# Kernel tuning notes

Hardware: AMD Instinct MI355X
Metric: run time of the kernel (lower is better)

The kernel has to match this reference:

```python
import jax, jax.numpy as jnp
import numpy as np

L_GNN = 4          # num_layers - 1
NUM_GRAPHS = 64
BN_EPS = 1e-5


def _bn(x, g, b):
    # torch BatchNorm1d in training mode: biased variance, per-feature affine
    m = x.mean(axis=0)
    v = ((x - m) ** 2).mean(axis=0)
    return g * (x - m) * jax.lax.rsqrt(v + BN_EPS) + b


def _mlp(x, W1, b1, g, bb, W2, b2):
    # GIN 2-layer MLP: Linear -> BN -> ReLU -> Linear
    h = jax.nn.relu(_bn(x @ W1 + b1, g, bb))
    return h @ W2 + b2


def setup_inputs():
    key = jax.random.key(0)
    ks = jax.random.split(key, 20)
    N1, N2, E1, E2 = 8192, 4096, 262144, 65536
    D1, D2, H, O = 128, 64, 512, 10

    def nrm(k, shape, scale=0.05):
        return (jax.random.normal(k, shape) * scale).astype(jnp.float32)

    return {
        "x1": jax.random.normal(ks[0], (N1, D1), jnp.float32),
        "x2": jax.random.normal(ks[1], (N2, D2), jnp.float32),
        "motif2A": jax.random.uniform(ks[2], (N2, N1), jnp.float32),
        "edge1": jax.random.randint(ks[3], (2, E1), 0, N1),
        "edge2": jax.random.randint(ks[4], (2, E2), 0, N2),
        "graph_ids": jnp.sort(jax.random.randint(ks[5], (N1,), 0, NUM_GRAPHS)),
        "eps": jnp.zeros((L_GNN,), jnp.float32),
        "atts": jax.random.uniform(ks[6], (2,), jnp.float32),
        "mlp1_W1_0": nrm(ks[7], (D1, H)),
        "mlp1_W1_rest": nrm(ks[8], (L_GNN - 1, 2 * H, H)),
        "mlp1_b1": jnp.zeros((L_GNN, H), jnp.float32),
        "mlp1_bn_g": jnp.ones((L_GNN, H), jnp.float32),
        "mlp1_bn_b": jnp.zeros((L_GNN, H), jnp.float32),
        "mlp1_W2": nrm(ks[9], (L_GNN, H, H)),
        "mlp1_b2": jnp.zeros((L_GNN, H), jnp.float32),
        "bn1_g": jnp.ones((L_GNN, H), jnp.float32),
        "bn1_b": jnp.zeros((L_GNN, H), jnp.float32),
        "mlp2_W1_0": nrm(ks[10], (D2, H)),
        "mlp2_W1_rest": nrm(ks[11], (L_GNN - 1, H, H)),
        "mlp2_b1": jnp.zeros((L_GNN, H), jnp.float32),
        "mlp2_bn_g": jnp.ones((L_GNN, H), jnp.float32),
        "mlp2_bn_b": jnp.zeros((L_GNN, H), jnp.float32),
        "mlp2_W2": nrm(ks[12], (L_GNN, H, H)),
        "mlp2_b2": jnp.zeros((L_GNN, H), jnp.float32),
        "bn2_g": jnp.ones((L_GNN, H), jnp.float32),
        "bn2_b": jnp.zeros((L_GNN, H), jnp.float32),
        "pred_W0": nrm(ks[13], (D1, O)),
        "pred_b0": jnp.zeros((O,), jnp.float32),
        "pred_W": nrm(ks[14], (L_GNN, 2 * H, O)),
        "pred_b": jnp.zeros((L_GNN, O), jnp.float32),
    }


def reference(x1, x2, motif2A, edge1, edge2, graph_ids, eps, atts,
              mlp1_W1_0, mlp1_W1_rest, mlp1_b1, mlp1_bn_g, mlp1_bn_b, mlp1_W2, mlp1_b2,
              bn1_g, bn1_b,
              mlp2_W1_0, mlp2_W1_rest, mlp2_b1, mlp2_bn_g, mlp2_bn_b, mlp2_W2, mlp2_b2,
              bn2_g, bn2_b,
              pred_W0, pred_b0, pred_W, pred_b):
    N1, N2 = x1.shape[0], x2.shape[0]
    a = jax.nn.softmax(atts)                      # attention over [self-graph, hyper-graph]
    h1, h2 = x1, x2
    hidden = [x1]
    for l in range(L_GNN):
        # spmm(Adj, h) == scatter-sum of source features onto destination rows
        pooled1 = jax.ops.segment_sum(h1[edge1[1]], edge1[0], num_segments=N1)
        pooled1 = pooled1 + (1.0 + eps[l]) * h1   # learn_eps branch (next_layer_eps)
        W1 = mlp1_W1_0 if l == 0 else mlp1_W1_rest[l - 1]
        rep1 = _mlp(pooled1, W1, mlp1_b1[l], mlp1_bn_g[l], mlp1_bn_b[l], mlp1_W2[l], mlp1_b2[l])
        h1 = jax.nn.relu(_bn(rep1, bn1_g[l], bn1_b[l]))
        # hyper graph branch
        pooled2 = jax.ops.segment_sum(h2[edge2[1]], edge2[0], num_segments=N2)
        pooled2 = pooled2 + (1.0 + eps[l]) * h2
        W1h = mlp2_W1_0 if l == 0 else mlp2_W1_rest[l - 1]
        rep2 = _mlp(pooled2, W1h, mlp2_b1[l], mlp2_bn_g[l], mlp2_bn_b[l], mlp2_W2[l], mlp2_b2[l])
        h2 = jax.nn.relu(_bn(rep2, bn2_g[l], bn2_b[l]))
        # project hyper-node features back to base nodes and fuse with attention
        h2A = motif2A.T @ h2                      # [N1, H]
        h1 = jnp.concatenate([a[0] * h1, a[1] * h2A], axis=1)  # [N1, 2H]
        hidden.append(h1)
    # jumping-knowledge readout: sum graph pooling + per-layer linear heads
    score = jax.ops.segment_sum(hidden[0], graph_ids, num_segments=NUM_GRAPHS) @ pred_W0 + pred_b0
    for l in range(L_GNN):
        pooled_h = jax.ops.segment_sum(hidden[l + 1], graph_ids, num_segments=NUM_GRAPHS)
        score = score + pooled_h @ pred_W[l] + pred_b[l]
    return score
```

## Files before the change

kernel.cpp:

```cpp
#include <hip/hip_runtime.h>

using bf16x8 = __attribute__((ext_vector_type(8))) short;
using f32x4  = __attribute__((ext_vector_type(4))) float;
using u16x4  = __attribute__((ext_vector_type(4))) unsigned short;
using u16x8  = __attribute__((ext_vector_type(8))) unsigned short;
using as3_void  = __attribute__((address_space(3))) void;
using as1_cvoid = const __attribute__((address_space(1))) void;

__device__ __forceinline__ unsigned short f2bf(float x) {
    union { float f; unsigned u; } v; v.f = x;
    unsigned r = v.u + 0x7FFFu + ((v.u >> 16) & 1u);
    return (unsigned short)(r >> 16);
}
__device__ __forceinline__ float bf2f(unsigned short h) {
    union { unsigned u; float f; } v; v.u = ((unsigned)h) << 16;
    return v.f;
}

__device__ __forceinline__ void xcd_remap(int& bx, int& n0) {
    int flat  = blockIdx.x + gridDim.x * blockIdx.y;
    int total = gridDim.x * gridDim.y;
    int swz   = (flat & 7) * (total >> 3) + (flat >> 3);
    bx = swz >> 2;
    n0 = (swz & 3) * 128;
}

#define GEMM_BODY(BM, A, Bt, K, KBEG, KEND)                                          \
    constexpr int WROWS = (BM) / 2;                                                  \
    constexpr int MI = WROWS / 16;                                                   \
    __shared__ __align__(16) unsigned short As[(BM) * 64];                           \
    __shared__ __align__(16) unsigned short Bs[128 * 64];                            \
    const int tid  = threadIdx.x;                                                    \
    const int lane = tid & 63, wave = tid >> 6;                                      \
    const int wr = wave >> 1, wc = wave & 1;                                         \
    const int rl = lane & 15, kg = lane >> 4;                                        \
    f32x4 acc[MI][4] = {};                                                           \
    for (int kt = (KBEG); kt < (KEND); kt += 64) {                                   \
        _Pragma("unroll")                                                            \
        for (int it = 0; it < (BM) / 32; ++it) {                                     \
            int slot = it * 256 + tid;                                               \
            int r = slot >> 3, c = slot & 7;                                         \
            int cg = c ^ (r & 7);                                                    \
            const unsigned short* ga = (A) + (size_t)(m0 + r) * (K) + (kt + cg * 8); \
            __builtin_amdgcn_global_load_lds((as1_cvoid*)ga, (as3_void*)(As + slot * 8), 16, 0, 0); \
        }                                                                            \
        _Pragma("unroll")                                                            \
        for (int it = 0; it < 4; ++it) {                                             \
            int slot = it * 256 + tid;                                               \
            int r = slot >> 3, c = slot & 7;                                         \
            int cg = c ^ (r & 7);                                                    \
            const unsigned short* gb = (Bt) + (size_t)(n0 + r) * (K) + (kt + cg * 8);\
            __builtin_amdgcn_global_load_lds((as1_cvoid*)gb, (as3_void*)(Bs + slot * 8), 16, 0, 0); \
        }                                                                            \
        __syncthreads();                                                             \
        _Pragma("unroll")                                                            \
        for (int kh = 0; kh < 2; ++kh) {                                             \
            bf16x8 a_[MI], b_[4];                                                    \
            _Pragma("unroll")                                                        \
            for (int i = 0; i < MI; ++i) {                                           \
                int ra = wr * WROWS + i * 16 + rl;                                   \
                int ca = (kh * 4 + kg) ^ (ra & 7);                                   \
                a_[i] = *reinterpret_cast<const bf16x8*>(&As[ra * 64 + ca * 8]);     \
            }                                                                        \
            _Pragma("unroll")                                                        \
            for (int j = 0; j < 4; ++j) {                                            \
                int rb = wc * 64 + j * 16 + rl;                                      \
                int cb = (kh * 4 + kg) ^ (rb & 7);                                   \
                b_[j] = *reinterpret_cast<const bf16x8*>(&Bs[rb * 64 + cb * 8]);     \
            }                                                                        \
            _Pragma("unroll")                                                        \
            for (int i = 0; i < MI; ++i)                                             \
                _Pragma("unroll")                                                    \
                for (int j = 0; j < 4; ++j)                                          \
                    acc[i][j] = __builtin_amdgcn_mfma_f32_16x16x32_bf16(a_[i], b_[j], acc[i][j], 0, 0, 0); \
        }                                                                            \
        __syncthreads();                                                             \
    }

__global__ __launch_bounds__(256) void gemm_dual(
    int nb0,
    const unsigned short* __restrict__ A0, const unsigned short* __restrict__ B0,
    int K0, unsigned short* __restrict__ C0, float* __restrict__ st0,
    const unsigned short* __restrict__ A1, const unsigned short* __restrict__ B1,
    int K1, unsigned short* __restrict__ C1, float* __restrict__ st1)
{
    int bx, n0;
    xcd_remap(bx, n0);
    const unsigned short *A, *Bt; unsigned short* Cb; float* statp;
    int K;
    if (bx < nb0) { A = A0; Bt = B0; K = K0; Cb = C0; statp = st0; }
    else { bx -= nb0; A = A1; Bt = B1; K = K1; Cb = C1; statp = st1; }
    const int m0 = bx * 64;

    GEMM_BODY(64, A, Bt, K, 0, K)

#pragma unroll
    for (int i = 0; i < MI; ++i)
#pragma unroll
        for (int j = 0; j < 4; ++j)
#pragma unroll
            for (int e = 0; e < 4; ++e) {
                int rr = m0 + wr * WROWS + i * 16 + kg * 4 + e;
                int cc = n0 + wc * 64 + j * 16 + rl;
                Cb[(size_t)rr * 512 + cc] = f2bf(acc[i][j][e]);
            }
    if (statp) {
#pragma unroll
        for (int j = 0; j < 4; ++j) {
            float s = 0.f, q = 0.f;
#pragma unroll
            for (int i = 0; i < MI; ++i)
#pragma unroll
                for (int e = 0; e < 4; ++e) {
                    float x = acc[i][j][e];
                    s += x; q += x * x;
                }
            s += __shfl_xor(s, 16); s += __shfl_xor(s, 32);
            q += __shfl_xor(q, 16); q += __shfl_xor(q, 32);
            if (kg == 0) {
                int cc = n0 + wc * 64 + j * 16 + rl;
                atomicAdd(&statp[cc], s);
                atomicAdd(&statp[512 + cc], q);
            }
        }
    }
}

__global__ __launch_bounds__(256) void gemm_splitk(
    const unsigned short* __restrict__ A, const unsigned short* __restrict__ Bt,
    int M, int N, int K, float* __restrict__ Cp)
{
    int bx, n0;
    xcd_remap(bx, n0);
    const int m0 = bx * 128;
    const int kn = K / gridDim.z, kbeg = blockIdx.z * kn;

    GEMM_BODY(128, A, Bt, K, kbeg, kbeg + kn)

    float* dst = Cp + (size_t)blockIdx.z * M * N;
#pragma unroll
    for (int i = 0; i < MI; ++i)
#pragma unroll
        for (int j = 0; j < 4; ++j)
#pragma unroll
            for (int e = 0; e < 4; ++e) {
                int rr = m0 + wr * WROWS + i * 16 + kg * 4 + e;
                int cc = n0 + wc * 64 + j * 16 + rl;
                dst[(size_t)rr * N + cc] = acc[i][j][e];
            }
}

__global__ void csr_count2(const int* __restrict__ e1, int E1, int* __restrict__ c1,
                           const int* __restrict__ e2, int E2, int* __restrict__ c2) {
    int i = blockIdx.x * 256 + threadIdx.x;
    if (i < E1) atomicAdd(&c1[e1[i]], 1);
    else if (i < E1 + E2) atomicAdd(&c2[e2[i - E1]], 1);
}

__global__ void csr_scan2(const int* __restrict__ cnt1, int n1, int* __restrict__ offs1, int* __restrict__ cur1,
                          const int* __restrict__ cnt2, int n2, int* __restrict__ offs2, int* __restrict__ cur2) {
    const int* cnt = blockIdx.x ? cnt2 : cnt1;
    int n           = blockIdx.x ? n2 : n1;
    int* offs       = blockIdx.x ? offs2 : offs1;
    int* cursor     = blockIdx.x ? cur2 : cur1;
    __shared__ int part[1024];
    int t = threadIdx.x;
    int per = n >> 10;
    int base = t * per;
    int loc[8];
    int s = 0;
    for (int j = 0; j < per; ++j) { loc[j] = s; s += cnt[base + j]; }
    part[t] = s;
    __syncthreads();
    for (int o = 1; o < 1024; o <<= 1) {
        int v = (t >= o) ? part[t - o] : 0;
        __syncthreads();
        part[t] += v;
        __syncthreads();
    }
    int excl = (t == 0) ? 0 : part[t - 1];
    for (int j = 0; j < per; ++j) {
        int v = excl + loc[j];
        offs[base + j] = v;
        cursor[base + j] = v;
    }
    if (t == 1023) offs[n] = part[1023];
}

__global__ void csr_fill2(const int* __restrict__ e1, int E1, int* __restrict__ cur1, int* __restrict__ s1,
                          const int* __restrict__ e2, int E2, int* __restrict__ cur2, int* __restrict__ s2) {
    int i = blockIdx.x * 256 + threadIdx.x;
    if (i < E1) {
        int d = e1[i], s = e1[E1 + i];
        s1[atomicAdd(&cur1[d], 1)] = s;
    } else if (i < E1 + E2) {
        int e = i - E1;
        int d = e2[e], s = e2[E2 + e];
        s2[atomicAdd(&cur2[d], 1)] = s;
    }
}

__global__ __launch_bounds__(128) void gather2_bf16(
    const u16x4* __restrict__ Y1, const int* __restrict__ offs1, const int* __restrict__ srcs1,
    u16x4* __restrict__ T1, int n1,
    const u16x4* __restrict__ Y2, const int* __restrict__ offs2, const int* __restrict__ srcs2,
    u16x4* __restrict__ T2,
    const float* __restrict__ epsv, int l)
{
    int i = blockIdx.x;
    const u16x4* Y; u16x4* T; const int *offs, *srcs;
    if (i < n1) { Y = Y1; T = T1; offs = offs1; srcs = srcs1; }
    else        { i -= n1; Y = Y2; T = T2; offs = offs2; srcs = srcs2; }
    int c = threadIdx.x;
    float e = 1.0f + epsv[l];
    int lo = offs[i], hi = offs[i + 1];
    u16x4 hv = Y[(size_t)i * 128 + c];
    f32x4 a0, a1 = {}, a2 = {}, a3 = {};
#pragma unroll
    for (int j = 0; j < 4; ++j) a0[j] = e * bf2f(hv[j]);
    int k = lo;
    for (; k + 4 <= hi; k += 4) {
        int s0 = srcs[k], s1 = srcs[k + 1], s2 = srcs[k + 2], s3 = srcs[k + 3];
        u16x4 v0 = Y[(size_t)s0 * 128 + c];
        u16x4 v1 = Y[(size_t)s1 * 128 + c];
        u16x4 v2 = Y[(size_t)s2 * 128 + c];
        u16x4 v3 = Y[(size_t)s3 * 128 + c];
#pragma unroll
        for (int j = 0; j < 4; ++j) {
            a0[j] += bf2f(v0[j]); a1[j] += bf2f(v1[j]);
            a2[j] += bf2f(v2[j]); a3[j] += bf2f(v3[j]);
        }
    }
    for (; k < hi; ++k) {
        u16x4 v = Y[(size_t)srcs[k] * 128 + c];
#pragma unroll
        for (int j = 0; j < 4; ++j) a0[j] += bf2f(v[j]);
    }
    f32x4 acc = (a0 + a1) + (a2 + a3);
    u16x4 o;
#pragma unroll
    for (int j = 0; j < 4; ++j) o[j] = f2bf(acc[j]);
    T[(size_t)i * 128 + c] = o;
}

__global__ __launch_bounds__(64) void gather2_l0(
    const u16x4* __restrict__ X1, const int* __restrict__ offs1, const int* __restrict__ srcs1,
    u16x4* __restrict__ T1, int n1,
    const u16x4* __restrict__ X2, const int* __restrict__ offs2, const int* __restrict__ srcs2,
    u16x4* __restrict__ T2,
    const float* __restrict__ epsv)
{
    int i = blockIdx.x;
    const u16x4* X; u16x4* T; const int *offs, *srcs; int nc4;
    if (i < n1) { X = X1; T = T1; offs = offs1; srcs = srcs1; nc4 = 32; }
    else        { i -= n1; X = X2; T = T2; offs = offs2; srcs = srcs2; nc4 = 16; }
    int c = threadIdx.x;
    if (c >= nc4) return;
    float e = 1.0f + epsv[0];
    int lo = offs[i], hi = offs[i + 1];
    u16x4 hv = X[(size_t)i * nc4 + c];
    f32x4 a0, a1 = {}, a2 = {}, a3 = {};
#pragma unroll
    for (int j = 0; j < 4; ++j) a0[j] = e * bf2f(hv[j]);
    int k = lo;
    for (; k + 4 <= hi; k += 4) {
        int s0 = srcs[k], s1 = srcs[k + 1], s2 = srcs[k + 2], s3 = srcs[k + 3];
        u16x4 v0 = X[(size_t)s0 * nc4 + c];
        u16x4 v1 = X[(size_t)s1 * nc4 + c];
        u16x4 v2 = X[(size_t)s2 * nc4 + c];
        u16x4 v3 = X[(size_t)s3 * nc4 + c];
#pragma unroll
        for (int j = 0; j < 4; ++j) {
            a0[j] += bf2f(v0[j]); a1[j] += bf2f(v1[j]);
            a2[j] += bf2f(v2[j]); a3[j] += bf2f(v3[j]);
        }
    }
    for (; k < hi; ++k) {
        u16x4 v = X[(size_t)srcs[k] * nc4 + c];
#pragma unroll
        for (int j = 0; j < 4; ++j) a0[j] += bf2f(v[j]);
    }
    f32x4 acc = (a0 + a1) + (a2 + a3);
    u16x4 o;
#pragma unroll
    for (int j = 0; j < 4; ++j) o[j] = f2bf(acc[j]);
    T[(size_t)i * nc4 + c] = o;
}

__global__ void bn_stats2(int nb0,
                          const u16x4* __restrict__ X0, float* __restrict__ ss0,
                          const u16x4* __restrict__ X1, float* __restrict__ ss1) {
    int bx = blockIdx.x;
    const u16x4* X; float* ss;
    if (bx < nb0) { X = X0; ss = ss0; }
    else { bx -= nb0; X = X1; ss = ss1; }
    int c = threadIdx.x;
    int r0 = bx * 16;
    f32x4 s = {}, q = {};
    for (int r = 0; r < 16; ++r) {
        u16x4 v = X[(size_t)(r0 + r) * 128 + c];
        f32x4 f;
#pragma unroll
        for (int j = 0; j < 4; ++j) f[j] = bf2f(v[j]);
        s += f; q += f * f;
    }
#pragma unroll
    for (int j = 0; j < 4; ++j) {
        atomicAdd(&ss[c * 4 + j], s[j]);
        atomicAdd(&ss[512 + c * 4 + j], q[j]);
    }
}

__global__ __launch_bounds__(128) void bn_apply_mid(
    int nb0,
    const u16x4* __restrict__ X0, int M0, const float* __restrict__ ss0,
    const float* __restrict__ g0, const float* __restrict__ b0, unsigned short* __restrict__ o0,
    const u16x4* __restrict__ X1, int M1, const float* __restrict__ ss1,
    const float* __restrict__ g1, const float* __restrict__ b1, unsigned short* __restrict__ o1)
{
    int bx = blockIdx.x;
    const u16x4* X; const float *ss, *g, *b; unsigned short* out; int M;
    if (bx < nb0) { X = X0; M = M0; ss = ss0; g = g0; b = b0; out = o0; }
    else { bx -= nb0; X = X1; M = M1; ss = ss1; g = g1; b = b1; out = o1; }
    int c = threadIdx.x;
    float inv = 1.0f / (float)M;
    float al[4], be[4];
#pragma unroll
    for (int i = 0; i < 4; ++i) {
        float mean = ss[c * 4 + i] * inv;
        float var  = ss[512 + c * 4 + i] * inv - mean * mean;
        al[i] = g[c * 4 + i] * rsqrtf(var + 1e-5f);
        be[i] = b[c * 4 + i] - mean * al[i];
    }
    int r0 = bx * 8;
    for (int r = 0; r < 8; ++r) {
        u16x4 v = X[(size_t)(r0 + r) * 128 + c];
        u16x4 h;
#pragma unroll
        for (int i = 0; i < 4; ++i)
            h[i] = f2bf(fmaxf(al[i] * bf2f(v[i]) + be[i], 0.f));
        *reinterpret_cast<u16x4*>(out + (size_t)(r0 + r) * 512 + c * 4) = h;
    }
}

__global__ __launch_bounds__(128) void bn_apply_b2t(
    const u16x4* __restrict__ X, int M, const float* __restrict__ ss,
    const float* __restrict__ g, const float* __restrict__ b,
    unsigned short* __restrict__ out, unsigned short* __restrict__ outT)
{
    int c = threadIdx.x;
    float inv = 1.0f / (float)M;
    float al[4], be[4];
#pragma unroll
    for (int i = 0; i < 4; ++i) {
        float mean = ss[c * 4 + i] * inv;
        float var  = ss[512 + c * 4 + i] * inv - mean * mean;
        al[i] = g[c * 4 + i] * rsqrtf(var + 1e-5f);
        be[i] = b[c * 4 + i] - mean * al[i];
    }
    int r0 = blockIdx.x * 8;
    u16x8 t8[4];
#pragma unroll
    for (int r = 0; r < 8; ++r) {
        u16x4 v = X[(size_t)(r0 + r) * 128 + c];
        u16x4 h;
#pragma unroll
        for (int i = 0; i < 4; ++i) {
            h[i] = f2bf(fmaxf(al[i] * bf2f(v[i]) + be[i], 0.f));
            t8[i][r] = h[i];
        }
        *reinterpret_cast<u16x4*>(out + (size_t)(r0 + r) * 512 + c * 4) = h;
    }
#pragma unroll
    for (int i = 0; i < 4; ++i)
        *reinterpret_cast<u16x8*>(outT + (size_t)(c * 4 + i) * 4096 + r0) = t8[i];
}

__global__ __launch_bounds__(128) void finale(
    int nb0, const int* __restrict__ gid, const float* __restrict__ aDev,
    float* __restrict__ pool, unsigned short* __restrict__ H1,
    const u16x4* __restrict__ X, const float* __restrict__ ss,
    const float* __restrict__ g, const float* __restrict__ b,
    const f32x4* __restrict__ P, int ks)
{
    int bx = blockIdx.x;
    int c = threadIdx.x;
    int job = bx >= nb0;
    if (job) bx -= nb0;
    int r0 = bx * 8;
    int ooff = job ? 512 : 0;
    float al[4], be[4];
    float sc;
    if (!job) {
        sc = aDev[0];
        float inv = 1.0f / 8192.0f;
#pragma unroll
        for (int i = 0; i < 4; ++i) {
            float mean = ss[c * 4 + i] * inv;
            float var  = ss[512 + c * 4 + i] * inv - mean * mean;
            al[i] = g[c * 4 + i] * rsqrtf(var + 1e-5f);
            be[i] = b[c * 4 + i] - mean * al[i];
        }
    } else {
        sc = aDev[1];
    }
    const int total4 = 8192 * 128;
    int curg = gid[r0];
    f32x4 pacc = {};
    for (int r = 0; r < 8; ++r) {
        int row = r0 + r;
        u16x4 h;
        f32x4 f;
        if (!job) {
            u16x4 v = X[(size_t)row * 128 + c];
#pragma unroll
            for (int i = 0; i < 4; ++i) {
                h[i] = f2bf(fmaxf(al[i] * bf2f(v[i]) + be[i], 0.f) * sc);
                f[i] = bf2f(h[i]);
            }
        } else {
            f32x4 s = P[(size_t)row * 128 + c];
            for (int z = 1; z < ks; ++z) s += P[(size_t)z * total4 + (size_t)row * 128 + c];
#pragma unroll
            for (int i = 0; i < 4; ++i) { h[i] = f2bf(s[i] * sc); f[i] = bf2f(h[i]); }
        }
        *reinterpret_cast<u16x4*>(H1 + (size_t)row * 1024 + ooff + c * 4) = h;
        int gg = gid[row];
        if (gg != curg) {
#pragma unroll
            for (int j = 0; j < 4; ++j)
                atomicAdd(&pool[(size_t)curg * 1024 + ooff + c * 4 + j], pacc[j]);
            pacc = {}; curg = gg;
        }
        pacc += f;
    }
#pragma unroll
    for (int j = 0; j < 4; ++j)
        atomicAdd(&pool[(size_t)curg * 1024 + ooff + c * 4 + j], pacc[j]);
}

__global__ void cvt2_bf16(const f32x4* __restrict__ X0, u16x4* __restrict__ O0, int n0,
                          const f32x4* __restrict__ X1, u16x4* __restrict__ O1, int n1) {
    for (int i = blockIdx.x * blockDim.x + threadIdx.x; i < n0 + n1; i += gridDim.x * blockDim.x) {
        const f32x4* X; u16x4* O; int k;
        if (i < n0) { X = X0; O = O0; k = i; }
        else { X = X1; O = O1; k = i - n0; }
        f32x4 v = X[k];
        u16x4 h;
#pragma unroll
        for (int j = 0; j < 4; ++j) h[j] = f2bf(v[j]);
        O[k] = h;
    }
}

__global__ __launch_bounds__(256) void motif_transpose(const float* __restrict__ S,
                                                       unsigned short* __restrict__ D) {
    __shared__ unsigned short tile[64][66];
    int m0 = blockIdx.x * 64;
    int k0 = blockIdx.y * 64;
    int t = threadIdx.x;
    int r = t >> 4, cq = t & 15;
#pragma unroll
    for (int p = 0; p < 4; ++p) {
        int row = r + p * 16;
        f32x4 v = *reinterpret_cast<const f32x4*>(S + (size_t)(k0 + row) * 8192 + m0 + cq * 4);
        u16x4 h;
#pragma unroll
        for (int j = 0; j < 4; ++j) h[j] = f2bf(v[j]);
        *reinterpret_cast<u16x4*>(&tile[row][cq * 4]) = h;
    }
    __syncthreads();
#pragma unroll
    for (int p = 0; p < 4; ++p) {
        int col = r + p * 16;
        u16x4 h;
#pragma unroll
        for (int i = 0; i < 4; ++i) h[i] = tile[cq * 4 + i][col];
        *reinterpret_cast<u16x4*>(D + (size_t)(m0 + col) * 4096 + k0 + cq * 4) = h;
    }
}

__global__ void transpose_cvt_b(const float* __restrict__ S, unsigned short* __restrict__ D,
                                int rows, int cols, size_t sstride, size_t dstride) {
    S += blockIdx.z * sstride; D += blockIdx.z * dstride;
    __shared__ unsigned short tile[32][33];
    int x0 = blockIdx.x * 32, y0 = blockIdx.y * 32;
    for (int j = threadIdx.y; j < 32; j += blockDim.y)
        tile[j][threadIdx.x] = f2bf(S[(size_t)(y0 + j) * cols + x0 + threadIdx.x]);
    __syncthreads();
    for (int j = threadIdx.y; j < 32; j += blockDim.y)
        D[(size_t)(x0 + j) * rows + y0 + threadIdx.x] = tile[threadIdx.x][j];
}

__global__ void transpose_cvt11(const float* __restrict__ A, unsigned short* __restrict__ Ad,
                                const float* __restrict__ B, unsigned short* __restrict__ Bd,
                                const float* __restrict__ Cs, unsigned short* __restrict__ Cd) {
    int z = blockIdx.z;
    const float* S; unsigned short* D;
    if (z < 4)      { S = A  + (size_t)z * 262144;       D = Ad + (size_t)z * 262144; }
    else if (z < 7) { S = B  + (size_t)(z - 4) * 262144; D = Bd + (size_t)(z - 4) * 262144; }
    else            { S = Cs + (size_t)(z - 7) * 262144; D = Cd + (size_t)(z - 7) * 262144; }
    __shared__ unsigned short tile[32][33];
    int x0 = blockIdx.x * 32, y0 = blockIdx.y * 32;
    for (int j = threadIdx.y; j < 32; j += blockDim.y)
        tile[j][threadIdx.x] = f2bf(S[(size_t)(y0 + j) * 512 + x0 + threadIdx.x]);
    __syncthreads();
    for (int j = threadIdx.y; j < 32; j += blockDim.y)
        D[(size_t)(x0 + j) * 512 + y0 + threadIdx.x] = tile[threadIdx.x][j];
}

__device__ __forceinline__ int lbound(const int* __restrict__ a, int n, int v) {
    int lo = 0, hi = n;
    while (lo < hi) { int m = (lo + hi) >> 1; if (a[m] < v) lo = m + 1; else hi = m; }
    return lo;
}

__global__ void pool_f32_at(const float* __restrict__ Hm, const int* __restrict__ gid,
                            int n, float* __restrict__ P) {
    int g = blockIdx.x;
    int lo = lbound(gid, n, g), hi = lbound(gid, n, g + 1);
    int cnt = hi - lo;
    int per = (cnt + 3) >> 2;
    int s = lo + blockIdx.y * per;
    int e = min(s + per, hi);
    if (s >= e) return;
    int c = threadIdx.x;
    f32x4 acc = {};
    for (int i = s; i < e; ++i)
        acc += *reinterpret_cast<const f32x4*>(Hm + (size_t)i * 128 + c * 4);
#pragma unroll
    for (int j = 0; j < 4; ++j)
        atomicAdd(&P[(size_t)g * 128 + c * 4 + j], acc[j]);
}

__global__ void softmax2(const float* __restrict__ atts, float* __restrict__ a) {
    if (threadIdx.x == 0) {
        float m = fmaxf(atts[0], atts[1]);
        float e0 = expf(atts[0] - m), e1 = expf(atts[1] - m);
        float inv = 1.0f / (e0 + e1);
        a[0] = e0 * inv; a[1] = e1 * inv;
    }
}

__global__ __launch_bounds__(256) void score_kernel(
    const float* __restrict__ P0, const float* __restrict__ PL,
    const float* __restrict__ W0, const float* __restrict__ b0,
    const float* __restrict__ W, const float* __restrict__ bb,
    float* __restrict__ out)
{
    int g = blockIdx.x;
    int t = threadIdx.x;
    float part[10];
#pragma unroll
    for (int o = 0; o < 10; ++o) part[o] = 0.f;
    if (t < 128) {
        float p = P0[g * 128 + t];
#pragma unroll
        for (int o = 0; o < 10; ++o) part[o] += p * W0[t * 10 + o];
    }
    for (int l = 0; l < 4; ++l) {
        const float* p = PL + (size_t)l * 65536 + (size_t)g * 1024;
        const float* w = W + (size_t)l * 10240;
        for (int k = t; k < 1024; k += 256) {
            float pv = p[k];
#pragma unroll
            for (int o = 0; o < 10; ++o) part[o] += pv * w[k * 10 + o];
        }
    }
    __shared__ float red[4][10];
#pragma unroll
    for (int o = 0; o < 10; ++o) {
        float v = part[o];
        for (int off = 32; off; off >>= 1) v += __shfl_down(v, off, 64);
        if ((t & 63) == 0) red[t >> 6][o] = v;
    }
    __syncthreads();
    if (t < 10) {
        float s = b0[t] + red[0][t] + red[1][t] + red[2][t] + red[3][t];
#pragma unroll
        for (int l = 0; l < 4; ++l) s += bb[l * 10 + t];
        out[g * 10 + t] = s;
    }
}

extern "C" void kernel_launch(void* const* d_in, const int* in_sizes, int n_in,
                              void* d_out, int out_size, void* d_ws, size_t ws_size,
                              hipStream_t stream) {
    const float* x1    = (const float*)d_in[0];
    const float* x2    = (const float*)d_in[1];
    const float* motif = (const float*)d_in[2];
    const int*   edge1 = (const int*)d_in[3];
    const int*   edge2 = (const int*)d_in[4];
    const int*   gid   = (const int*)d_in[5];
    const float* epsv  = (const float*)d_in[6];
    const float* atts  = (const float*)d_in[7];
    const float* m1W10 = (const float*)d_in[8];
    const float* m1W1r = (const float*)d_in[9];
    const float* m1bng = (const float*)d_in[11];
    const float* m1bnb = (const float*)d_in[12];
    const float* m1W2  = (const float*)d_in[13];
    const float* bn1g  = (const float*)d_in[15];
    const float* bn1b  = (const float*)d_in[16];
    const float* m2W10 = (const float*)d_in[17];
    const float* m2W1r = (const float*)d_in[18];
    const float* m2bng = (const float*)d_in[20];
    const float* m2bnb = (const float*)d_in[21];
    const float* m2W2  = (const float*)d_in[22];
    const float* bn2g  = (const float*)d_in[24];
    const float* bn2b  = (const float*)d_in[25];
    const float* pW0   = (const float*)d_in[26];
    const float* pb0   = (const float*)d_in[27];
    const float* pW    = (const float*)d_in[28];
    const float* pb    = (const float*)d_in[29];
    float* out = (float*)d_out;

    constexpr int N1 = 8192, N2 = 4096, E1 = 262144, E2 = 65536;

    char* base = (char*)d_ws;
    size_t off = 0;
    auto alloc = [&](size_t bytes) -> void* {
        void* p = base + off;
        off = (off + bytes + 255) & ~(size_t)255;
        return p;
    };

    unsigned short* motifT  = (unsigned short*)alloc((size_t)8192 * 4096 * 2);
    unsigned short* w1t1_0  = (unsigned short*)alloc((size_t)512 * 128 * 2);
    unsigned short* w1t1_r  = (unsigned short*)alloc((size_t)3 * 512 * 1024 * 2);
    unsigned short* w2t1    = (unsigned short*)alloc((size_t)4 * 512 * 512 * 2);
    unsigned short* w1t2_0  = (unsigned short*)alloc((size_t)512 * 64 * 2);
    unsigned short* w1t2_r  = (unsigned short*)alloc((size_t)3 * 512 * 512 * 2);
    unsigned short* w2t2    = (unsigned short*)alloc((size_t)4 * 512 * 512 * 2);
    unsigned short* x1b     = (unsigned short*)alloc((size_t)N1 * 128 * 2);
    unsigned short* x2b     = (unsigned short*)alloc((size_t)N2 * 64 * 2);
    unsigned short* Tx1     = (unsigned short*)alloc((size_t)N1 * 128 * 2);
    unsigned short* Tx2     = (unsigned short*)alloc((size_t)N2 * 64 * 2);
    unsigned short* H1b     = (unsigned short*)alloc((size_t)N1 * 1024 * 2);
    unsigned short* H2b     = (unsigned short*)alloc((size_t)N2 * 512 * 2);
    unsigned short* H2t     = (unsigned short*)alloc((size_t)512 * 4096 * 2);
    unsigned short* U1b     = (unsigned short*)alloc((size_t)N1 * 512 * 2);
    unsigned short* U2b     = (unsigned short*)alloc((size_t)N2 * 512 * 2);
    unsigned short* Y1b     = (unsigned short*)alloc((size_t)N1 * 512 * 2);
    unsigned short* T1b     = (unsigned short*)alloc((size_t)N1 * 512 * 2);
    unsigned short* Y2b     = (unsigned short*)alloc((size_t)N2 * 512 * 2);
    unsigned short* T2b     = (unsigned short*)alloc((size_t)N2 * 512 * 2);
    int*   cnt1 = (int*)alloc((size_t)N1 * 4);
    int*   cnt2 = (int*)alloc((size_t)N2 * 4);
    float* ss   = (float*)alloc((size_t)16 * 1024 * 4);
    float* PL   = (float*)alloc((size_t)4 * 64 * 1024 * 4);
    float* P0   = (float*)alloc((size_t)64 * 128 * 4);
    const size_t zero_bytes = (size_t)N1 * 4 + N2 * 4 + 16 * 1024 * 4 + 4 * 64 * 1024 * 4
                            + 64 * 128 * 4;
    int*   offs1 = (int*)alloc((size_t)(N1 + 1) * 4);
    int*   offs2 = (int*)alloc((size_t)(N2 + 1) * 4);
    int*   cur1  = (int*)alloc((size_t)N1 * 4);
    int*   cur2  = (int*)alloc((size_t)N2 * 4);
    int*   srcs1 = (int*)alloc((size_t)E1 * 4);
    int*   srcs2 = (int*)alloc((size_t)E2 * 4);
    float* aDev  = (float*)alloc(256);

    if (off > ws_size) return;

    const size_t part_elems = (size_t)N1 * 512;
    size_t rem = ws_size - off;
    int KS = (rem >= 4 * part_elems * 4) ? 4 : (rem >= 2 * part_elems * 4) ? 2 : 1;
    float* Cpart = (float*)(base + off);

    hipMemsetAsync(cnt1, 0, zero_bytes, stream);
    softmax2<<<1, 64, 0, stream>>>(atts, aDev);
    cvt2_bf16<<<512, 256, 0, stream>>>((const f32x4*)x1, (u16x4*)x1b, N1 * 128 / 4,
                                       (const f32x4*)x2, (u16x4*)x2b, N2 * 64 / 4);
    motif_transpose<<<dim3(128, 64), 256, 0, stream>>>(motif, motifT);
    transpose_cvt_b<<<dim3(16, 4, 1), dim3(32, 8), 0, stream>>>(m1W10, w1t1_0, 128, 512, 0, 0);
    transpose_cvt_b<<<dim3(16, 32, 3), dim3(32, 8), 0, stream>>>(m1W1r, w1t1_r, 1024, 512,
                                                                 (size_t)1024 * 512, (size_t)512 * 1024);
    transpose_cvt_b<<<dim3(16, 2, 1), dim3(32, 8), 0, stream>>>(m2W10, w1t2_0, 64, 512, 0, 0);
    transpose_cvt11<<<dim3(16, 16, 11), dim3(32, 8), 0, stream>>>(m1W2, w2t1, m2W1r, w1t2_r, m2W2, w2t2);
    csr_count2<<<(E1 + E2) / 256, 256, 0, stream>>>(edge1, E1, cnt1, edge2, E2, cnt2);
    csr_scan2<<<2, 1024, 0, stream>>>(cnt1, N1, offs1, cur1, cnt2, N2, offs2, cur2);
    csr_fill2<<<(E1 + E2) / 256, 256, 0, stream>>>(edge1, E1, cur1, srcs1, edge2, E2, cur2, srcs2);
    pool_f32_at<<<dim3(64, 4), 32, 0, stream>>>(x1, gid, N1, P0);

    for (int l = 0; l < 4; ++l) {
        float* ssl = ss + (size_t)l * 4096;
        float* PLl = PL + (size_t)l * 65536;
        if (l == 0) {
            gather2_l0<<<N1 + N2, 64, 0, stream>>>(
                (const u16x4*)x1b, offs1, srcs1, (u16x4*)Tx1, N1,
                (const u16x4*)x2b, offs2, srcs2, (u16x4*)Tx2, epsv);
            gemm_dual<<<dim3(192, 4), 256, 0, stream>>>(
                128,
                Tx1, w1t1_0, 128, T1b, ssl + 0 * 1024,
                Tx2, w1t2_0, 64,  T2b, ssl + 2 * 1024);
        } else {
            gemm_dual<<<dim3(192, 4), 256, 0, stream>>>(
                128,
                H1b, w1t1_r + (size_t)(l - 1) * 512 * 1024, 1024, Y1b, nullptr,
                H2b, w1t2_r + (size_t)(l - 1) * 512 * 512,  512,  Y2b, nullptr);
            gather2_bf16<<<N1 + N2, 128, 0, stream>>>(
                (const u16x4*)Y1b, offs1, srcs1, (u16x4*)T1b, N1,
                (const u16x4*)Y2b, offs2, srcs2, (u16x4*)T2b, epsv, l);
            bn_stats2<<<768, 128, 0, stream>>>(512, (const u16x4*)T1b, ssl + 0 * 1024,
                                               (const u16x4*)T2b, ssl + 2 * 1024);
        }
        bn_apply_mid<<<1536, 128, 0, stream>>>(
            1024,
            (const u16x4*)T1b, N1, ssl + 0 * 1024, m1bng + l * 512, m1bnb + l * 512, U1b,
            (const u16x4*)T2b, N2, ssl + 2 * 1024, m2bng + l * 512, m2bnb + l * 512, U2b);
        gemm_dual<<<dim3(192, 4), 256, 0, stream>>>(
            128,
            U1b, w2t1 + (size_t)l * 512 * 512, 512, Y1b, ssl + 1 * 1024,
            U2b, w2t2 + (size_t)l * 512 * 512, 512, Y2b, ssl + 3 * 1024);
        bn_apply_b2t<<<512, 128, 0, stream>>>(
            (const u16x4*)Y2b, N2, ssl + 3 * 1024, bn2g + l * 512, bn2b + l * 512, H2b, H2t);
        gemm_splitk<<<dim3(64, 4, KS), 256, 0, stream>>>(motifT, H2t, N1, 512, 4096, Cpart);
        finale<<<2048, 128, 0, stream>>>(
            1024, gid, aDev, PLl, H1b,
            (const u16x4*)Y1b, ssl + 1 * 1024, bn1g + l * 512, bn1b + l * 512,
            (const f32x4*)Cpart, KS);
    }

    score_kernel<<<64, 256, 0, stream>>>(P0, PL, pW0, pb0, pW, pb, out);
}
```

Before: 916.4 us.

## Skip last-layer motif GEMM by reassociating pooled readout through prediction weights

On the final layer the projected hyper-node features only feed the graph-sum readout. That readout equals the pooled transposed motif matrix times h2 times the head weights, so the code precomputes per-graph pooled motif rows (Pm) once. It also forms V = a1 * h2 @ W_head for the last layer and folds Pm @ V into the score kernel. This removes the large split-K motif GEMM and half of the finale work in layer 3, at the cost of an extra pooling kernel over motifT, a small GEMV kernel, and a larger score reduction.

After: 902.8 us. About the same (-1.5%).

```diff
diff --git a/kernel.cpp b/kernel.cpp
--- a/kernel.cpp
+++ b/kernel.cpp
@@ -371,9 +371,11 @@
         }
         *reinterpret_cast<u16x4*>(out + (size_t)(r0 + r) * 512 + c * 4) = h;
     }
-#pragma unroll
-    for (int i = 0; i < 4; ++i)
-        *reinterpret_cast<u16x8*>(outT + (size_t)(c * 4 + i) * 4096 + r0) = t8[i];
+    if (outT) {
+#pragma unroll
+        for (int i = 0; i < 4; ++i)
+            *reinterpret_cast<u16x8*>(outT + (size_t)(c * 4 + i) * 4096 + r0) = t8[i];
+    }
 }
 
 __global__ __launch_bounds__(128) void finale(
@@ -533,6 +535,43 @@
         atomicAdd(&P[(size_t)g * 128 + c * 4 + j], acc[j]);
 }
 
+__global__ __launch_bounds__(128) void pool_pm(const u16x4* __restrict__ Mt,
+                                               const int* __restrict__ gid,
+                                               float* __restrict__ Pm) {
+    int g = blockIdx.x;
+    int lo = lbound(gid, 8192, g), hi = lbound(gid, 8192, g + 1);
+    int c = blockIdx.y * 128 + threadIdx.x;
+    f32x4 acc = {};
+    for (int i = lo; i < hi; ++i) {
+        u16x4 v = Mt[(size_t)i * 1024 + c];
+#pragma unroll
+        for (int j = 0; j < 4; ++j) acc[j] += bf2f(v[j]);
+    }
+    *reinterpret_cast<f32x4*>(Pm + (size_t)g * 4096 + (size_t)c * 4) = acc;
+}
+
+__global__ __launch_bounds__(256) void v_kernel(
+    const unsigned short* __restrict__ H2, const float* __restrict__ Wb,
+    const float* __restrict__ aDev, float* __restrict__ V) {
+    int w = threadIdx.x >> 6, l = threadIdx.x & 63;
+    int k = blockIdx.x * 4 + w;
+    float part[10];
+#pragma unroll
+    for (int o = 0; o < 10; ++o) part[o] = 0.f;
+    for (int c = l; c < 512; c += 64) {
+        float v = bf2f(H2[(size_t)k * 512 + c]);
+#pragma unroll
+        for (int o = 0; o < 10; ++o) part[o] += v * Wb[c * 10 + o];
+    }
+    float a1 = aDev[1];
+#pragma unroll
+    for (int o = 0; o < 10; ++o) {
+        float v = part[o];
+        for (int off = 32; off; off >>= 1) v += __shfl_down(v, off, 64);
+        if (l == 0) V[(size_t)k * 10 + o] = a1 * v;
+    }
+}
+
 __global__ void softmax2(const float* __restrict__ atts, float* __restrict__ a) {
     if (threadIdx.x == 0) {
         float m = fmaxf(atts[0], atts[1]);
@@ -546,6 +585,7 @@
     const float* __restrict__ P0, const float* __restrict__ PL,
     const float* __restrict__ W0, const float* __restrict__ b0,
     const float* __restrict__ W, const float* __restrict__ bb,
+    const float* __restrict__ Pm, const float* __restrict__ V,
     float* __restrict__ out)
 {
     int g = blockIdx.x;
@@ -566,6 +606,11 @@
 #pragma unroll
             for (int o = 0; o < 10; ++o) part[o] += pv * w[k * 10 + o];
         }
+    }
+    for (int k = t; k < 4096; k += 256) {
+        float pv = Pm[(size_t)g * 4096 + k];
+#pragma unroll
+        for (int o = 0; o < 10; ++o) part[o] += pv * V[(size_t)k * 10 + o];
     }
     __shared__ float red[4][10];
 #pragma unroll
@@ -657,6 +702,8 @@
     int*   cur2  = (int*)alloc((size_t)N2 * 4);
     int*   srcs1 = (int*)alloc((size_t)E1 * 4);
     int*   srcs2 = (int*)alloc((size_t)E2 * 4);
+    float* Pm    = (float*)alloc((size_t)64 * 4096 * 4);
+    float* Vbuf  = (float*)alloc((size_t)4096 * 10 * 4);
     float* aDev  = (float*)alloc(256);
 
     if (off > ws_size) return;
@@ -671,6 +718,7 @@
     cvt2_bf16<<<512, 256, 0, stream>>>((const f32x4*)x1, (u16x4*)x1b, N1 * 128 / 4,
                                        (const f32x4*)x2, (u16x4*)x2b, N2 * 64 / 4);
     motif_transpose<<<dim3(128, 64), 256, 0, stream>>>(motif, motifT);
+    pool_pm<<<dim3(64, 8), 128, 0, stream>>>((const u16x4*)motifT, gid, Pm);
     transpose_cvt_b<<<dim3(16, 4, 1), dim3(32, 8), 0, stream>>>(m1W10, w1t1_0, 128, 512, 0, 0);
     transpose_cvt_b<<<dim3(16, 32, 3), dim3(32, 8), 0, stream>>>(m1W1r, w1t1_r, 1024, 512,
                                                                  (size_t)1024 * 512, (size_t)512 * 1024);
@@ -711,14 +759,25 @@
             128,
             U1b, w2t1 + (size_t)l * 512 * 512, 512, Y1b, ssl + 1 * 1024,
             U2b, w2t2 + (size_t)l * 512 * 512, 512, Y2b, ssl + 3 * 1024);
-        bn_apply_b2t<<<512, 128, 0, stream>>>(
-            (const u16x4*)Y2b, N2, ssl + 3 * 1024, bn2g + l * 512, bn2b + l * 512, H2b, H2t);
-        gemm_splitk<<<dim3(64, 4, KS), 256, 0, stream>>>(motifT, H2t, N1, 512, 4096, Cpart);
-        finale<<<2048, 128, 0, stream>>>(
-            1024, gid, aDev, PLl, H1b,
-            (const u16x4*)Y1b, ssl + 1 * 1024, bn1g + l * 512, bn1b + l * 512,
-            (const f32x4*)Cpart, KS);
-    }
-
-    score_kernel<<<64, 256, 0, stream>>>(P0, PL, pW0, pb0, pW, pb, out);
-}
+        if (l < 3) {
+            bn_apply_b2t<<<512, 128, 0, stream>>>(
+                (const u16x4*)Y2b, N2, ssl + 3 * 1024, bn2g + l * 512, bn2b + l * 512, H2b, H2t);
+            gemm_splitk<<<dim3(64, 4, KS), 256, 0, stream>>>(motifT, H2t, N1, 512, 4096, Cpart);
+            finale<<<2048, 128, 0, stream>>>(
+                1024, gid, aDev, PLl, H1b,
+                (const u16x4*)Y1b, ssl + 1 * 1024, bn1g + l * 512, bn1b + l * 512,
+                (const f32x4*)Cpart, KS);
+        } else {
+            bn_apply_b2t<<<512, 128, 0, stream>>>(
+                (const u16x4*)Y2b, N2, ssl + 3 * 1024, bn2g + l * 512, bn2b + l * 512,
+                H2b, nullptr);
+            v_kernel<<<1024, 256, 0, stream>>>(H2b, pW + 3 * 10240 + 512 * 10, aDev, Vbuf);
+            finale<<<1024, 128, 0, stream>>>(
+                1024, gid, aDev, PLl, H1b,
+                (const u16x4*)Y1b, ssl + 1 * 1024, bn1g + l * 512, bn1b + l * 512,
+                (const f32x4*)Cpart, KS);
+        }
+    }
+
+    score_kernel<<<64, 256, 0, stream>>>(P0, PL, pW0, pb0, pW, pb, Pm, Vbuf, out);
+}
```
